# Kernel optimization log

Hardware: AMD Instinct MI355X
Metric: run time of the kernel (lower is better)

## Reference

```python
import jax, jax.numpy as jnp
import numpy as np

V = 5000      # output_class_dim
E = 512       # embed_dim
F = 512       # 2 * listener_hidden_dim
H = 512       # speller_hidden_dim
HEADS = 4
HD = F // HEADS  # 128
STEPS = 64    # max_label_len
B, T = 32, 1024


def setup_inputs() -> dict:
    key = jax.random.key(0)
    ks = jax.random.split(key, 10)
    s = 0.05
    return {
        "listener_feature": jax.random.normal(ks[0], (B, T, F), jnp.float32),
        "embedding": jax.random.normal(ks[1], (V, E), jnp.float32) * s,
        # LSTM cell (single layer, torch gate order i,f,g,o)
        "W_ih": jax.random.normal(ks[2], (4 * H, E + F), jnp.float32) * s,
        "W_hh": jax.random.normal(ks[3], (4 * H, H), jnp.float32) * s,
        "b_ih": jax.random.normal(ks[4], (4 * H,), jnp.float32) * s,
        "b_hh": jax.random.normal(ks[5], (4 * H,), jnp.float32) * s,
        # predict_hid: Linear(2H -> 512)
        "Wp": jax.random.normal(ks[6], (512, 2 * H), jnp.float32) * s,
        "bp": jax.random.normal(ks[7], (512,), jnp.float32) * s,
        # character_distribution: Linear(512 -> V)
        "Wc": jax.random.normal(ks[8], (V, 512), jnp.float32) * s,
        "bc": jax.random.normal(ks[9], (V,), jnp.float32) * s,
    }


def _decode(listener_feature, embedding, W_ih, W_hh, b_ih, b_hh, Wp, bp, Wc, bc):
    b = listener_feature.shape[0]
    lf_heads = listener_feature.reshape(b, T, HEADS, HD)  # [B,T,h,d]

    def lstm_cell(x, h, c):
        gates = x @ W_ih.T + h @ W_hh.T + (b_ih + b_hh)
        i, f, g, o = jnp.split(gates, 4, axis=-1)
        c_new = jax.nn.sigmoid(f) * c + jax.nn.sigmoid(i) * jnp.tanh(g)
        h_new = jax.nn.sigmoid(o) * jnp.tanh(c_new)
        return h_new, c_new

    def step(carry, _):
        h, c, rnn_in = carry
        h, c = lstm_cell(rnn_in, h, c)                       # rnn_output = h [B,H]
        ds = h.reshape(b, HEADS, HD)                          # decoder state per head
        energy = jnp.einsum('bhd,bthd->bht', ds, lf_heads)    # dot attention
        scores = jax.nn.softmax(energy, axis=-1)              # [B,h,T]
        context = jnp.einsum('bht,bthd->bhd', scores, lf_heads).reshape(b, F)
        concat = jnp.concatenate([h, context], axis=-1)       # [B,2H]
        hid = jnp.maximum(concat @ Wp.T + bp, 0.0)            # ReLU MLP
        raw_pred = jax.nn.log_softmax(hid @ Wc.T + bc, axis=-1)
        # greedy feedback (teacher_force_rate = 0 since ground_truth is None)
        tok = jnp.argmax(raw_pred, axis=-1)                   # [B]
        rnn_in_next = jnp.concatenate([embedding[tok], context], axis=-1)
        return (h, c, rnn_in_next), (raw_pred, scores[:, -1, :])

    h0 = jnp.zeros((b, H), listener_feature.dtype)
    c0 = jnp.zeros((b, H), listener_feature.dtype)
    # initial input: embedding of token 0, concat first listener frame
    emb0 = jnp.broadcast_to(embedding[0], (b, E))
    rnn_in0 = jnp.concatenate([emb0, listener_feature[:, 0, :]], axis=-1)

    _, (raw_pred_seq, attn_seq) = jax.lax.scan(step, (h0, c0, rnn_in0), None, length=STEPS)
    return raw_pred_seq, attn_seq  # [S,B,V], [S,B,T] (last head, as in original)


def reference(listener_feature, embedding, W_ih, W_hh, b_ih, b_hh, Wp, bp, Wc, bc):
    return _decode(listener_feature, embedding, W_ih, W_hh, b_ih, b_hh, Wp, bp, Wc, bc)
```

## Files before the change

### kernel.cpp

```cpp
#include <hip/hip_runtime.h>
#include <math.h>
#include <stdint.h>


#define NB 512
#define NT 256

constexpr int Tv = 1024, Vv = 5000, STEPS = 64;

constexpr int MCNT = 0;
constexpr int GEN  = 16;
constexpr int GCNT = 64;
constexpr int GFLG = 1024;
constexpr int ACNT = 2048;
constexpr int LCNT = 2560;
constexpr int WSU  = 4096;

constexpr int XH   = 0;
constexpr int HB   = XH + 32*1024;
constexpr int HID  = HB + 2*32*512;
constexpr int PART = HID + 32*512;
constexpr int E3   = PART + 32*4*16*130;
constexpr int PM   = E3 + 32*1024;
constexpr int PSUM = PM + 32*256;
constexpr int PIDX = PSUM + 32*256;
constexpr int MLS  = PIDX + 32*256;

__device__ __forceinline__ float sigm(float x) { return 1.f / (1.f + expf(-x)); }

__device__ __forceinline__ float ld4(const float* p) {
  return __hip_atomic_load(const_cast<float*>(p), __ATOMIC_RELAXED, __HIP_MEMORY_SCOPE_AGENT);
}
__device__ __forceinline__ float2 ld8(const float* p) {
  unsigned long long u = __hip_atomic_load(
      reinterpret_cast<unsigned long long*>(const_cast<float*>(p)),
      __ATOMIC_RELAXED, __HIP_MEMORY_SCOPE_AGENT);
  union { unsigned long long u; float2 f; } c; c.u = u; return c.f;
}
__device__ __forceinline__ int ld4i(const int* p) {
  return (int)__hip_atomic_load(reinterpret_cast<unsigned*>(const_cast<int*>(p)),
                                __ATOMIC_RELAXED, __HIP_MEMORY_SCOPE_AGENT);
}
__device__ __forceinline__ void st4(float* p, float v) {
  __hip_atomic_store(p, v, __ATOMIC_RELAXED, __HIP_MEMORY_SCOPE_AGENT);
}
__device__ __forceinline__ void st8(float* p, float2 v) {
  union { float2 f; unsigned long long u; } c; c.f = v;
  __hip_atomic_store(reinterpret_cast<unsigned long long*>(p), c.u,
                     __ATOMIC_RELAXED, __HIP_MEMORY_SCOPE_AGENT);
}
__device__ __forceinline__ void st4i(int* p, int v) {
  __hip_atomic_store(reinterpret_cast<unsigned*>(p), (unsigned)v,
                     __ATOMIC_RELAXED, __HIP_MEMORY_SCOPE_AGENT);
}
__device__ __forceinline__ unsigned ld_rlx(unsigned* p) {
  return __hip_atomic_load(p, __ATOMIC_RELAXED, __HIP_MEMORY_SCOPE_AGENT);
}
__device__ __forceinline__ void st_rlx(unsigned* p, unsigned v) {
  __hip_atomic_store(p, v, __ATOMIC_RELAXED, __HIP_MEMORY_SCOPE_AGENT);
}
__device__ __forceinline__ unsigned add_rlx(unsigned* p, unsigned v) {
  return __hip_atomic_fetch_add(p, v, __ATOMIC_RELAXED, __HIP_MEMORY_SCOPE_AGENT);
}

__device__ __forceinline__ void gsync(unsigned* wsu, int blk, int tid, unsigned& myGen) {
  __syncthreads();
  if (tid == 0) {
    const unsigned target = ++myGen;
    const int grp = blk >> 4;
    unsigned o = add_rlx(&wsu[GCNT + grp*16], 1u);
    if (o == target*16u - 1u) {
      unsigned o2 = add_rlx(&wsu[MCNT], 1u);
      if (o2 == target*32u - 1u) st_rlx(&wsu[GEN], target);
    }
    if ((blk & 15) == 0) {
      while (ld_rlx(&wsu[GEN]) != target) __builtin_amdgcn_s_sleep(8);
      st_rlx(&wsu[GFLG + grp*32], target);
    } else {
      while (ld_rlx(&wsu[GFLG + grp*32]) != target) __builtin_amdgcn_s_sleep(8);
    }
  }
  __syncthreads();
}

__global__ void speller_init(const float* __restrict__ LF, const float* __restrict__ Emb,
                             float* __restrict__ wsf, unsigned* __restrict__ wsu) {
  int b = blockIdx.x;
  for (int i = threadIdx.x; i < 512; i += NT) {
    st4(wsf + XH + b*1024 + i,       Emb[i]);
    st4(wsf + XH + b*1024 + 512 + i, LF[(size_t)b*Tv*512 + i]);
    st4(wsf + HB + b*512 + i,        0.f);
  }
  if (b == 0) for (int i = threadIdx.x; i < WSU; i += NT) st_rlx(wsu + i, 0u);
}

struct LdsA { float Wg[8][1536]; float Wpg[2][1536]; float gb[8]; float bpg[2]; };
struct LdsB { float Wc[20][512]; float bcl[20]; };
union  LdsU { LdsA a; LdsB b; };

__device__ __forceinline__ void gate_accum_A(float acc[8][2], float accW[2][2],
                                             const float* __restrict__ wsf,
                                             const float (&Wg)[8][1536],
                                             const float (&Wpg)[2][1536],
                                             int ks, int b0, int hbuf) {
#pragma unroll 2
  for (int q = 0; q < 8; ++q) {
    const int k4 = 512 + (q*16 + ks)*4;
    float2 xa[2], xb[2];
#pragma unroll
    for (int i = 0; i < 2; ++i) {
      const float* p = wsf + XH + (size_t)(b0+i)*1024 + k4;
      xa[i] = ld8(p); xb[i] = ld8(p + 2);
    }
#pragma unroll
    for (int r = 0; r < 8; ++r) {
      float4 wv = *(const float4*)(&Wg[r][k4]);
#pragma unroll
      for (int i = 0; i < 2; ++i)
        acc[r][i] += wv.x*xa[i].x + wv.y*xa[i].y + wv.z*xb[i].x + wv.w*xb[i].y;
    }
#pragma unroll
    for (int r = 0; r < 2; ++r) {
      float4 wv = *(const float4*)(&Wpg[r][k4]);
#pragma unroll
      for (int i = 0; i < 2; ++i)
        accW[r][i] += wv.x*xa[i].x + wv.y*xa[i].y + wv.z*xb[i].x + wv.w*xb[i].y;
    }
  }
#pragma unroll 2
  for (int q = 0; q < 8; ++q) {
    const int k4 = (q*16 + ks)*4;
    float2 xa[2], xb[2];
#pragma unroll
    for (int i = 0; i < 2; ++i) {
      const float* p = wsf + HB + hbuf*16384 + (size_t)(b0+i)*512 + k4;
      xa[i] = ld8(p); xb[i] = ld8(p + 2);
    }
#pragma unroll
    for (int r = 0; r < 8; ++r) {
      float4 wv = *(const float4*)(&Wg[r][1024 + k4]);
#pragma unroll
      for (int i = 0; i < 2; ++i)
        acc[r][i] += wv.x*xa[i].x + wv.y*xa[i].y + wv.z*xb[i].x + wv.w*xb[i].y;
    }
#pragma unroll
    for (int r = 0; r < 2; ++r) {
      float4 wv = *(const float4*)(&Wpg[r][1024 + k4]);
#pragma unroll
      for (int i = 0; i < 2; ++i)
        accW[r][i] += wv.x*xa[i].x + wv.y*xa[i].y + wv.z*xb[i].x + wv.w*xb[i].y;
    }
  }
}

__launch_bounds__(NT, 2)
__global__ void speller_main(const float* __restrict__ LF, const float* __restrict__ Emb,
                             const float* __restrict__ Wih, const float* __restrict__ Whh,
                             const float* __restrict__ bih, const float* __restrict__ bhh,
                             const float* __restrict__ Wp,  const float* __restrict__ bp,
                             const float* __restrict__ Wc,  const float* __restrict__ bc,
                             float* __restrict__ out, unsigned* __restrict__ wsu,
                             float* __restrict__ wsf) {
  const int blk = blockIdx.x, tid = threadIdx.x;
  unsigned myGen = 0;
  __shared__ LdsU lds;
  __shared__ float scr[784];
  __shared__ int  sint[300];

  const int ab = blk >> 4, atc = blk & 15;
  const int aw = tid >> 6, aln = tid & 63;

  float4 lfr[32];
  {
    const float4* src = (const float4*)(LF +
        (((size_t)ab*Tv + atc*64 + aln)*512 + aw*128));
#pragma unroll
    for (int q = 0; q < 32; ++q) lfr[q] = src[q];
  }

  if (blk < 256) {
    const int u0 = blk * 2;
    for (int idx = tid; idx < 8*1536; idx += NT) {
      int r = idx / 1536, k = idx - r*1536;
      int g = r >> 1, uu = r & 1;
      int row = g*512 + u0 + uu;
      lds.a.Wg[r][k] = (k < 1024) ? Wih[(size_t)row*1024 + k]
                                  : Whh[(size_t)row*512 + (k-1024)];
    }
    for (int idx = tid; idx < 2*1536; idx += NT) {
      int r = idx / 1536, k = idx - r*1536;
      float v = 0.f;
      if (k >= 512) v = (k < 1024) ? Wp[(size_t)(u0+r)*1024 + k]
                                   : Wp[(size_t)(u0+r)*1024 + (k-1024)];
      lds.a.Wpg[r][k] = v;
    }
    if (tid < 8) {
      int g = tid >> 1, uu = tid & 1, row = g*512 + u0 + uu;
      lds.a.gb[tid] = bih[row] + bhh[row];
    }
    if (tid < 2) lds.a.bpg[tid] = bp[u0 + tid];
  } else {
    const int blk2 = blk - 256, v0 = blk2*20;
    if (v0 < Vv) {
      for (int idx = tid; idx < 20*512; idx += NT) {
        int vi = idx >> 9, k = idx & 511;
        lds.b.Wc[vi][k] = Wc[(size_t)(v0+vi)*512 + k];
      }
      if (tid < 20) lds.b.bcl[tid] = bc[v0+tid];
    }
  }
  __syncthreads();

  float acc[8][2];
  float accW[2][2];
  float c_reg[2][2];
#pragma unroll
  for (int uu = 0; uu < 2; ++uu)
#pragma unroll
    for (int i = 0; i < 2; ++i) c_reg[uu][i] = 0.f;
  float lgv[20];

  if (blk < 256) {
    const int ks = tid & 15, b0 = (tid >> 4) * 2;
#pragma unroll
    for (int r = 0; r < 8; ++r)
#pragma unroll
      for (int i = 0; i < 2; ++i) acc[r][i] = 0.f;
#pragma unroll
    for (int r = 0; r < 2; ++r)
#pragma unroll
      for (int i = 0; i < 2; ++i) accW[r][i] = 0.f;
    gate_accum_A(acc, accW, wsf, lds.a.Wg, lds.a.Wpg, ks, b0, 0);
  }

#pragma unroll 1
  for (int s = 0; s < STEPS; ++s) {
    const int wbuf = (s + 1) & 1;

    if (blk < 256) {
      const int u0 = blk * 2;
      const int ks = tid & 15, b0 = (tid >> 4) * 2;
#pragma unroll 2
      for (int q = 0; q < 8; ++q) {
        const int k4 = (q*16 + ks)*4;
        float2 xa[2], xb[2];
#pragma unroll
        for (int i = 0; i < 2; ++i) {
          const float* p = wsf + XH + (size_t)(b0+i)*1024 + k4;
          xa[i] = ld8(p); xb[i] = ld8(p + 2);
        }
#pragma unroll
        for (int r = 0; r < 8; ++r) {
          float4 wv = *(const float4*)(&lds.a.Wg[r][k4]);
#pragma unroll
          for (int i = 0; i < 2; ++i)
            acc[r][i] += wv.x*xa[i].x + wv.y*xa[i].y + wv.z*xb[i].x + wv.w*xb[i].y;
        }
      }
#pragma unroll
      for (int r = 0; r < 8; ++r)
#pragma unroll
        for (int i = 0; i < 2; ++i) {
          float v = acc[r][i];
          v += __shfl_xor(v, 8); v += __shfl_xor(v, 4);
          v += __shfl_xor(v, 2); v += __shfl_xor(v, 1);
          acc[r][i] = v + lds.a.gb[r];
        }
      float hnew[2][2];
#pragma unroll
      for (int uu = 0; uu < 2; ++uu)
#pragma unroll
        for (int i = 0; i < 2; ++i) {
          float cn = sigm(acc[2+uu][i]) * c_reg[uu][i]
                   + sigm(acc[uu][i]) * tanhf(acc[4+uu][i]);
          c_reg[uu][i] = cn;
          hnew[uu][i] = sigm(acc[6+uu][i]) * tanhf(cn);
        }
      if (ks == 0) {
#pragma unroll
        for (int i = 0; i < 2; ++i)
          st8(wsf + HB + wbuf*16384 + (size_t)(b0+i)*512 + u0,
              make_float2(hnew[0][i], hnew[1][i]));
      }
    } else if (s > 0) {
      const int blk2 = blk - 256;
      if (blk2 < 250) {
        const int v0 = blk2 * 20, bb = tid >> 3, ks = tid & 7;
        if (ks == 0) {
          float2 ml = ld8(wsf + MLS + 2*bb);
          float sub = ml.x + ml.y;
#pragma unroll
          for (int vi = 0; vi < 20; ++vi)
            out[(size_t)(s-1)*160000 + (size_t)bb*5000 + v0 + vi] = lgv[vi] - sub;
        }
      }
    }
    gsync(wsu, blk, tid, myGen);

    {
      float* hs = scr;
      {
        float2 hv = ld8(wsf + HB + wbuf*16384 + (size_t)ab*512 + tid*2);
        hs[tid*2] = hv.x; hs[tid*2+1] = hv.y;
      }
      __syncthreads();
      float e = 0.f;
      {
        const float4* hp = (const float4*)(hs + aw*128);
#pragma unroll
        for (int q = 0; q < 32; ++q) {
          float4 f = lfr[q], hh = hp[q];
          e += f.x*hh.x + f.y*hh.y + f.z*hh.z + f.w*hh.w;
        }
      }
      float m = e;
#pragma unroll
      for (int off = 32; off; off >>= 1) m = fmaxf(m, __shfl_xor(m, off));
      float p = expf(e - m);
      float l = p;
#pragma unroll
      for (int off = 32; off; off >>= 1) l += __shfl_xor(l, off);
      if (aw == 3) st4(wsf + E3 + (size_t)ab*1024 + atc*64 + aln, e);
      float* pr = wsf + PART + (size_t)((ab*4 + aw)*16 + atc)*130;
#pragma unroll
      for (int ch = 0; ch < 2; ++ch) {
        float c[64];
#pragma unroll
        for (int q = 0; q < 16; ++q) {
          float4 f = lfr[ch*16 + q];
          c[4*q+0] = p*f.x; c[4*q+1] = p*f.y; c[4*q+2] = p*f.z; c[4*q+3] = p*f.w;
        }
#pragma unroll
        for (int o = 32; o >= 1; o >>= 1) {
#pragma unroll
          for (int j = 0; j < 32; ++j) {
            if (j < o) {
              float keep = (aln & o) ? c[j + o] : c[j];
              float send = (aln & o) ? c[j] : c[j + o];
              c[j] = keep + __shfl_xor(send, o);
            }
          }
        }
        st4(pr + 2 + ch*64 + aln, c[0]);
      }
      if (aln == 0) st8(pr, make_float2(m, l));
      __syncthreads();
      if (tid == 0) {
        unsigned old = add_rlx(&wsu[ACNT + ab*16], 1u);
        sint[0] = (old == (unsigned)(s*16 + 15));
      }
      __syncthreads();
      if (sint[0]) {
        const int w2 = tid >> 6, ln2 = tid & 63;
        const float* pb = wsf + PART + (size_t)(ab*4 + w2)*16*130;
        float M = -1e30f;
        float mv[16], lv[16];
#pragma unroll
        for (int i = 0; i < 16; ++i) { float2 t = ld8(pb + i*130); mv[i] = t.x; lv[i] = t.y; M = fmaxf(M, t.x); }
        float L = 0.f;
        float sc[16];
#pragma unroll
        for (int i = 0; i < 16; ++i) { sc[i] = expf(mv[i] - M); L += lv[i] * sc[i]; }
        float cc0 = 0.f, cc1 = 0.f;
#pragma unroll
        for (int i = 0; i < 16; ++i) {
          float2 cx = ld8(pb + i*130 + 2 + 2*ln2);
          cc0 += sc[i]*cx.x; cc1 += sc[i]*cx.y;
        }
        float invL = 1.f / L;
        st8(wsf + XH + (size_t)ab*1024 + 512 + w2*128 + 2*ln2,
            make_float2(cc0*invL, cc1*invL));
        if (ln2 == 0) { scr[768 + w2*2] = M; scr[769 + w2*2] = L; }
        __syncthreads();
        float M3 = scr[768 + 6], iL3 = 1.f / scr[768 + 7];
        for (int i = tid; i < 1024; i += NT)
          out[(size_t)10240000 + ((size_t)(s*32 + ab))*1024 + i] =
              expf(ld4(wsf + E3 + (size_t)ab*1024 + i) - M3) * iL3;
      }
    }
    gsync(wsu, blk, tid, myGen);

    if (blk < 256) {
      const int ks = tid & 15, b0 = (tid >> 4) * 2;
#pragma unroll
      for (int r = 0; r < 8; ++r)
#pragma unroll
        for (int i = 0; i < 2; ++i) acc[r][i] = 0.f;
#pragma unroll
      for (int r = 0; r < 2; ++r)
#pragma unroll
        for (int i = 0; i < 2; ++i) accW[r][i] = 0.f;
      gate_accum_A(acc, accW, wsf, lds.a.Wg, lds.a.Wpg, ks, b0, wbuf);
#pragma unroll
      for (int r = 0; r < 2; ++r)
#pragma unroll
        for (int i = 0; i < 2; ++i) {
          float v = accW[r][i];
          v += __shfl_xor(v, 8); v += __shfl_xor(v, 4);
          v += __shfl_xor(v, 2); v += __shfl_xor(v, 1);
          accW[r][i] = v + lds.a.bpg[r];
        }
      if (ks == 0) {
#pragma unroll
        for (int i = 0; i < 2; ++i)
          st8(wsf + HID + (size_t)(b0+i)*512 + blk*2,
              make_float2(fmaxf(accW[0][i], 0.f), fmaxf(accW[1][i], 0.f)));
      }
    }
    gsync(wsu, blk, tid, myGen);

    if (blk >= 256) {
      const int blk2 = blk - 256;
      if (blk2 < 250) {
        const int v0 = blk2 * 20;
        const int bb = tid >> 3, ks = tid & 7;
#pragma unroll
        for (int vi = 0; vi < 20; ++vi) lgv[vi] = 0.f;
        const float* hb = wsf + HID + (size_t)bb*512;
#pragma unroll 1
        for (int half = 0; half < 2; ++half) {
          float4 xr[8];
#pragma unroll
          for (int q = 0; q < 8; ++q) {
            const float* p = hb + ((half*8 + q)*8 + ks)*4;
            float2 a = ld8(p), b2v = ld8(p + 2);
            xr[q] = make_float4(a.x, a.y, b2v.x, b2v.y);
          }
#pragma unroll
          for (int vi = 0; vi < 20; ++vi) {
            float a = 0.f;
#pragma unroll
            for (int q = 0; q < 8; ++q) {
              float4 wv = *(const float4*)(&lds.b.Wc[vi][((half*8 + q)*8 + ks)*4]);
              a += wv.x*xr[q].x + wv.y*xr[q].y + wv.z*xr[q].z + wv.w*xr[q].w;
            }
            lgv[vi] += a;
          }
        }
#pragma unroll
        for (int vi = 0; vi < 20; ++vi) {
          float a = lgv[vi];
          a += __shfl_xor(a, 1); a += __shfl_xor(a, 2); a += __shfl_xor(a, 4);
          lgv[vi] = a + lds.b.bcl[vi];
        }
        float mych = lgv[0]; int ami = 0;
#pragma unroll
        for (int vi = 1; vi < 20; ++vi)
          if (lgv[vi] > mych) { mych = lgv[vi]; ami = vi; }
        float sume = 0.f;
#pragma unroll
        for (int vi = 0; vi < 20; ++vi) sume += expf(lgv[vi] - mych);
        if (ks == 0) {
          st4(wsf + PM + bb*256 + blk2, mych);
          st4(wsf + PSUM + bb*256 + blk2, sume);
          st4i((int*)(wsf + PIDX) + bb*256 + blk2, v0 + ami);
        }
      }
      __syncthreads();
      if (tid == 0 && blk2 < 250) add_rlx(&wsu[LCNT], 1u);
      if (blk2 < 32) {
        const int b2 = blk2;
        if (tid == 0) {
          while (ld_rlx(&wsu[LCNT]) < (unsigned)((s + 1) * 250))
            __builtin_amdgcn_s_sleep(8);
        }
        __syncthreads();
        float mv = -1e30f, sv = 0.f; int iv = 0x7fffffff;
        if (tid < 250) {
          mv = ld4(wsf + PM + b2*256 + tid);
          sv = ld4(wsf + PSUM + b2*256 + tid);
          iv = ld4i((const int*)(wsf + PIDX) + b2*256 + tid);
        }
        scr[tid] = mv; sint[40 + tid] = iv;
        __syncthreads();
        for (int off = 128; off; off >>= 1) {
          if (tid < off) {
            float m2 = scr[tid + off]; int i2 = sint[40 + tid + off];
            if (m2 > scr[tid] || (m2 == scr[tid] && i2 < sint[40 + tid])) {
              scr[tid] = m2; sint[40 + tid] = i2;
            }
          }
          __syncthreads();
        }
        float M = scr[0]; int tok = sint[40];
        __syncthreads();
        scr[tid] = sv * expf(mv - M);
        __syncthreads();
        for (int off = 128; off; off >>= 1) {
          if (tid < off) scr[tid] += scr[tid + off];
          __syncthreads();
        }
        if (tid == 0) st8(wsf + MLS + 2*b2, make_float2(M, logf(scr[0])));
        for (int i = tid; i < 256; i += NT) {
          const float2* er = (const float2*)(Emb + (size_t)tok*512);
          st8(wsf + XH + (size_t)b2*1024 + 2*i, er[i]);
        }
      }
    }
    gsync(wsu, blk, tid, myGen);
  }

  if (blk >= 256) {
    const int blk2 = blk - 256;
    if (blk2 < 250) {
      const int v0 = blk2 * 20, bb = tid >> 3, ks = tid & 7;
      if (ks == 0) {
        float2 ml = ld8(wsf + MLS + 2*bb);
        float sub = ml.x + ml.y;
#pragma unroll
        for (int vi = 0; vi < 20; ++vi)
          out[(size_t)63*160000 + (size_t)bb*5000 + v0 + vi] = lgv[vi] - sub;
      }
    }
  }
}

extern "C" void kernel_launch(void* const* d_in, const int* in_sizes, int n_in,
                              void* d_out, int out_size, void* d_ws, size_t ws_size,
                              hipStream_t stream) {
  (void)in_sizes; (void)n_in; (void)out_size; (void)ws_size;
  const float* LF  = (const float*)d_in[0];
  const float* Emb = (const float*)d_in[1];
  const float* Wih = (const float*)d_in[2];
  const float* Whh = (const float*)d_in[3];
  const float* bih = (const float*)d_in[4];
  const float* bhh = (const float*)d_in[5];
  const float* Wp  = (const float*)d_in[6];
  const float* bp  = (const float*)d_in[7];
  const float* Wc  = (const float*)d_in[8];
  const float* bc  = (const float*)d_in[9];
  float* out = (float*)d_out;
  unsigned* wsu = (unsigned*)d_ws;
  float* wsf = (float*)d_ws + WSU;

  speller_init<<<32, NT, 0, stream>>>(LF, Emb, wsf, wsu);
  speller_main<<<NB, NT, 0, stream>>>(LF, Emb, Wih, Whh, bih, bhh, Wp, bp, Wc, bc,
                                      out, wsu, wsf);
}
```

Measured before the change: 5.857 ms.

## Halve persistent grid to 256 blocks of 512 threads, doubling per-block work

```diff
diff --git a/kernel.cpp b/kernel.cpp
--- a/kernel.cpp
+++ b/kernel.cpp
@@ -3,8 +3,8 @@
 #include <stdint.h>
 
 
-#define NB 512
-#define NT 256
+#define NB 256
+#define NT 512
 
 constexpr int Tv = 1024, Vv = 5000, STEPS = 64;
 
@@ -71,7 +71,7 @@
     unsigned o = add_rlx(&wsu[GCNT + grp*16], 1u);
     if (o == target*16u - 1u) {
       unsigned o2 = add_rlx(&wsu[MCNT], 1u);
-      if (o2 == target*32u - 1u) st_rlx(&wsu[GEN], target);
+      if (o2 == target*16u - 1u) st_rlx(&wsu[GEN], target);
     }
     if ((blk & 15) == 0) {
       while (ld_rlx(&wsu[GEN]) != target) __builtin_amdgcn_s_sleep(8);
@@ -86,74 +86,58 @@
 __global__ void speller_init(const float* __restrict__ LF, const float* __restrict__ Emb,
                              float* __restrict__ wsf, unsigned* __restrict__ wsu) {
   int b = blockIdx.x;
-  for (int i = threadIdx.x; i < 512; i += NT) {
+  for (int i = threadIdx.x; i < 512; i += 256) {
     st4(wsf + XH + b*1024 + i,       Emb[i]);
     st4(wsf + XH + b*1024 + 512 + i, LF[(size_t)b*Tv*512 + i]);
     st4(wsf + HB + b*512 + i,        0.f);
   }
-  if (b == 0) for (int i = threadIdx.x; i < WSU; i += NT) st_rlx(wsu + i, 0u);
-}
-
-struct LdsA { float Wg[8][1536]; float Wpg[2][1536]; float gb[8]; float bpg[2]; };
-struct LdsB { float Wc[20][512]; float bcl[20]; };
+  if (b == 0) for (int i = threadIdx.x; i < WSU; i += 256) st_rlx(wsu + i, 0u);
+}
+
+struct LdsA { float Wg[16][1536]; float Wpg[4][1536]; float gb[16]; float bpg[4]; };
+struct LdsB { float Wc[40][512]; float bcl[40]; };
 union  LdsU { LdsA a; LdsB b; };
 
-__device__ __forceinline__ void gate_accum_A(float acc[8][2], float accW[2][2],
+__device__ __forceinline__ void gate_accum_A(float acc[16], float accW[4],
                                              const float* __restrict__ wsf,
-                                             const float (&Wg)[8][1536],
-                                             const float (&Wpg)[2][1536],
-                                             int ks, int b0, int hbuf) {
+                                             const float (&Wg)[16][1536],
+                                             const float (&Wpg)[4][1536],
+                                             int ks, int b, int hbuf) {
 #pragma unroll 2
   for (int q = 0; q < 8; ++q) {
     const int k4 = 512 + (q*16 + ks)*4;
-    float2 xa[2], xb[2];
-#pragma unroll
-    for (int i = 0; i < 2; ++i) {
-      const float* p = wsf + XH + (size_t)(b0+i)*1024 + k4;
-      xa[i] = ld8(p); xb[i] = ld8(p + 2);
-    }
-#pragma unroll
-    for (int r = 0; r < 8; ++r) {
+    const float* p = wsf + XH + (size_t)b*1024 + k4;
+    float2 xa = ld8(p), xb = ld8(p + 2);
+#pragma unroll
+    for (int r = 0; r < 16; ++r) {
       float4 wv = *(const float4*)(&Wg[r][k4]);
-#pragma unroll
-      for (int i = 0; i < 2; ++i)
-        acc[r][i] += wv.x*xa[i].x + wv.y*xa[i].y + wv.z*xb[i].x + wv.w*xb[i].y;
-    }
-#pragma unroll
-    for (int r = 0; r < 2; ++r) {
+      acc[r] += wv.x*xa.x + wv.y*xa.y + wv.z*xb.x + wv.w*xb.y;
+    }
+#pragma unroll
+    for (int r = 0; r < 4; ++r) {
       float4 wv = *(const float4*)(&Wpg[r][k4]);
-#pragma unroll
-      for (int i = 0; i < 2; ++i)
-        accW[r][i] += wv.x*xa[i].x + wv.y*xa[i].y + wv.z*xb[i].x + wv.w*xb[i].y;
+      accW[r] += wv.x*xa.x + wv.y*xa.y + wv.z*xb.x + wv.w*xb.y;
     }
   }
 #pragma unroll 2
   for (int q = 0; q < 8; ++q) {
     const int k4 = (q*16 + ks)*4;
-    float2 xa[2], xb[2];
-#pragma unroll
-    for (int i = 0; i < 2; ++i) {
-      const float* p = wsf + HB + hbuf*16384 + (size_t)(b0+i)*512 + k4;
-      xa[i] = ld8(p); xb[i] = ld8(p + 2);
-    }
-#pragma unroll
-    for (int r = 0; r < 8; ++r) {
+    const float* p = wsf + HB + hbuf*16384 + (size_t)b*512 + k4;
+    float2 xa = ld8(p), xb = ld8(p + 2);
+#pragma unroll
+    for (int r = 0; r < 16; ++r) {
       float4 wv = *(const float4*)(&Wg[r][1024 + k4]);
-#pragma unroll
-      for (int i = 0; i < 2; ++i)
-        acc[r][i] += wv.x*xa[i].x + wv.y*xa[i].y + wv.z*xb[i].x + wv.w*xb[i].y;
-    }
-#pragma unroll
-    for (int r = 0; r < 2; ++r) {
+      acc[r] += wv.x*xa.x + wv.y*xa.y + wv.z*xb.x + wv.w*xb.y;
+    }
+#pragma unroll
+    for (int r = 0; r < 4; ++r) {
       float4 wv = *(const float4*)(&Wpg[r][1024 + k4]);
-#pragma unroll
-      for (int i = 0; i < 2; ++i)
-        accW[r][i] += wv.x*xa[i].x + wv.y*xa[i].y + wv.z*xb[i].x + wv.w*xb[i].y;
-    }
-  }
-}
-
-__launch_bounds__(NT, 2)
+      accW[r] += wv.x*xa.x + wv.y*xa.y + wv.z*xb.x + wv.w*xb.y;
+    }
+  }
+}
+
+__launch_bounds__(NT, 1)
 __global__ void speller_main(const float* __restrict__ LF, const float* __restrict__ Emb,
                              const float* __restrict__ Wih, const float* __restrict__ Whh,
                              const float* __restrict__ bih, const float* __restrict__ bhh,
@@ -167,8 +151,10 @@
   __shared__ float scr[784];
   __shared__ int  sint[300];
 
-  const int ab = blk >> 4, atc = blk & 15;
-  const int aw = tid >> 6, aln = tid & 63;
+  const int ab  = blk >> 3;
+  const int wavid = tid >> 6, aln = tid & 63;
+  const int aw  = wavid & 3, sub = wavid >> 2;
+  const int atc = (blk & 7)*2 + sub;
 
   float4 lfr[32];
   {
@@ -178,120 +164,104 @@
     for (int q = 0; q < 32; ++q) lfr[q] = src[q];
   }
 
-  if (blk < 256) {
-    const int u0 = blk * 2;
-    for (int idx = tid; idx < 8*1536; idx += NT) {
+  if (blk < 128) {
+    const int u0 = blk * 4;
+    for (int idx = tid; idx < 16*1536; idx += NT) {
       int r = idx / 1536, k = idx - r*1536;
-      int g = r >> 1, uu = r & 1;
+      int g = r >> 2, uu = r & 3;
       int row = g*512 + u0 + uu;
       lds.a.Wg[r][k] = (k < 1024) ? Wih[(size_t)row*1024 + k]
                                   : Whh[(size_t)row*512 + (k-1024)];
     }
-    for (int idx = tid; idx < 2*1536; idx += NT) {
+    for (int idx = tid; idx < 4*1536; idx += NT) {
       int r = idx / 1536, k = idx - r*1536;
       float v = 0.f;
       if (k >= 512) v = (k < 1024) ? Wp[(size_t)(u0+r)*1024 + k]
                                    : Wp[(size_t)(u0+r)*1024 + (k-1024)];
       lds.a.Wpg[r][k] = v;
     }
-    if (tid < 8) {
-      int g = tid >> 1, uu = tid & 1, row = g*512 + u0 + uu;
+    if (tid < 16) {
+      int g = tid >> 2, uu = tid & 3, row = g*512 + u0 + uu;
       lds.a.gb[tid] = bih[row] + bhh[row];
     }
-    if (tid < 2) lds.a.bpg[tid] = bp[u0 + tid];
+    if (tid < 4) lds.a.bpg[tid] = bp[u0 + tid];
   } else {
-    const int blk2 = blk - 256, v0 = blk2*20;
-    if (v0 < Vv) {
-      for (int idx = tid; idx < 20*512; idx += NT) {
+    const int blk2 = blk - 128, v0 = blk2*40;
+    if (blk2 < 125) {
+      for (int idx = tid; idx < 40*512; idx += NT) {
         int vi = idx >> 9, k = idx & 511;
         lds.b.Wc[vi][k] = Wc[(size_t)(v0+vi)*512 + k];
       }
-      if (tid < 20) lds.b.bcl[tid] = bc[v0+tid];
+      if (tid < 40) lds.b.bcl[tid] = bc[v0+tid];
     }
   }
   __syncthreads();
 
-  float acc[8][2];
-  float accW[2][2];
-  float c_reg[2][2];
-#pragma unroll
-  for (int uu = 0; uu < 2; ++uu)
-#pragma unroll
-    for (int i = 0; i < 2; ++i) c_reg[uu][i] = 0.f;
-  float lgv[20];
-
-  if (blk < 256) {
-    const int ks = tid & 15, b0 = (tid >> 4) * 2;
-#pragma unroll
-    for (int r = 0; r < 8; ++r)
-#pragma unroll
-      for (int i = 0; i < 2; ++i) acc[r][i] = 0.f;
-#pragma unroll
-    for (int r = 0; r < 2; ++r)
-#pragma unroll
-      for (int i = 0; i < 2; ++i) accW[r][i] = 0.f;
-    gate_accum_A(acc, accW, wsf, lds.a.Wg, lds.a.Wpg, ks, b0, 0);
+  float acc[16];
+  float accW[4];
+  float c_reg[4];
+#pragma unroll
+  for (int uu = 0; uu < 4; ++uu) c_reg[uu] = 0.f;
+  float lgv[40];
+
+  if (blk < 128) {
+    const int ks = tid & 15, b = tid >> 4;
+#pragma unroll
+    for (int r = 0; r < 16; ++r) acc[r] = 0.f;
+#pragma unroll
+    for (int r = 0; r < 4; ++r) accW[r] = 0.f;
+    gate_accum_A(acc, accW, wsf, lds.a.Wg, lds.a.Wpg, ks, b, 0);
   }
 
 #pragma unroll 1
   for (int s = 0; s < STEPS; ++s) {
     const int wbuf = (s + 1) & 1;
 
-    if (blk < 256) {
-      const int u0 = blk * 2;
-      const int ks = tid & 15, b0 = (tid >> 4) * 2;
+    if (blk < 128) {
+      const int u0 = blk * 4;
+      const int ks = tid & 15, b = tid >> 4;
 #pragma unroll 2
       for (int q = 0; q < 8; ++q) {
         const int k4 = (q*16 + ks)*4;
-        float2 xa[2], xb[2];
-#pragma unroll
-        for (int i = 0; i < 2; ++i) {
-          const float* p = wsf + XH + (size_t)(b0+i)*1024 + k4;
-          xa[i] = ld8(p); xb[i] = ld8(p + 2);
-        }
-#pragma unroll
-        for (int r = 0; r < 8; ++r) {
+        const float* p = wsf + XH + (size_t)b*1024 + k4;
+        float2 xa = ld8(p), xb = ld8(p + 2);
+#pragma unroll
+        for (int r = 0; r < 16; ++r) {
           float4 wv = *(const float4*)(&lds.a.Wg[r][k4]);
-#pragma unroll
-          for (int i = 0; i < 2; ++i)
-            acc[r][i] += wv.x*xa[i].x + wv.y*xa[i].y + wv.z*xb[i].x + wv.w*xb[i].y;
-        }
-      }
-#pragma unroll
-      for (int r = 0; r < 8; ++r)
-#pragma unroll
-        for (int i = 0; i < 2; ++i) {
-          float v = acc[r][i];
-          v += __shfl_xor(v, 8); v += __shfl_xor(v, 4);
-          v += __shfl_xor(v, 2); v += __shfl_xor(v, 1);
-          acc[r][i] = v + lds.a.gb[r];
-        }
-      float hnew[2][2];
-#pragma unroll
-      for (int uu = 0; uu < 2; ++uu)
-#pragma unroll
-        for (int i = 0; i < 2; ++i) {
-          float cn = sigm(acc[2+uu][i]) * c_reg[uu][i]
-                   + sigm(acc[uu][i]) * tanhf(acc[4+uu][i]);
-          c_reg[uu][i] = cn;
-          hnew[uu][i] = sigm(acc[6+uu][i]) * tanhf(cn);
-        }
+          acc[r] += wv.x*xa.x + wv.y*xa.y + wv.z*xb.x + wv.w*xb.y;
+        }
+      }
+#pragma unroll
+      for (int r = 0; r < 16; ++r) {
+        float v = acc[r];
+        v += __shfl_xor(v, 8); v += __shfl_xor(v, 4);
+        v += __shfl_xor(v, 2); v += __shfl_xor(v, 1);
+        acc[r] = v + lds.a.gb[r];
+      }
+      float hnew[4];
+#pragma unroll
+      for (int uu = 0; uu < 4; ++uu) {
+        float cn = sigm(acc[4+uu]) * c_reg[uu]
+                 + sigm(acc[uu]) * tanhf(acc[8+uu]);
+        c_reg[uu] = cn;
+        hnew[uu] = sigm(acc[12+uu]) * tanhf(cn);
+      }
       if (ks == 0) {
-#pragma unroll
-        for (int i = 0; i < 2; ++i)
-          st8(wsf + HB + wbuf*16384 + (size_t)(b0+i)*512 + u0,
-              make_float2(hnew[0][i], hnew[1][i]));
+        st8(wsf + HB + wbuf*16384 + (size_t)b*512 + u0,
+            make_float2(hnew[0], hnew[1]));
+        st8(wsf + HB + wbuf*16384 + (size_t)b*512 + u0 + 2,
+            make_float2(hnew[2], hnew[3]));
       }
     } else if (s > 0) {
-      const int blk2 = blk - 256;
-      if (blk2 < 250) {
-        const int v0 = blk2 * 20, bb = tid >> 3, ks = tid & 7;
+      const int blk2 = blk - 128;
+      if (blk2 < 125) {
+        const int v0 = blk2 * 40, bb = tid >> 4, ks = tid & 15;
         if (ks == 0) {
           float2 ml = ld8(wsf + MLS + 2*bb);
-          float sub = ml.x + ml.y;
-#pragma unroll
-          for (int vi = 0; vi < 20; ++vi)
-            out[(size_t)(s-1)*160000 + (size_t)bb*5000 + v0 + vi] = lgv[vi] - sub;
+          float sub2 = ml.x + ml.y;
+#pragma unroll
+          for (int vi = 0; vi < 40; ++vi)
+            out[(size_t)(s-1)*160000 + (size_t)bb*5000 + v0 + vi] = lgv[vi] - sub2;
         }
       }
     }
@@ -299,7 +269,7 @@
 
     {
       float* hs = scr;
-      {
+      if (tid < 256) {
         float2 hv = ld8(wsf + HB + wbuf*16384 + (size_t)ab*512 + tid*2);
         hs[tid*2] = hv.x; hs[tid*2+1] = hv.y;
       }
@@ -347,30 +317,32 @@
       __syncthreads();
       if (tid == 0) {
         unsigned old = add_rlx(&wsu[ACNT + ab*16], 1u);
-        sint[0] = (old == (unsigned)(s*16 + 15));
+        sint[0] = (old == (unsigned)(s*8 + 7));
       }
       __syncthreads();
       if (sint[0]) {
-        const int w2 = tid >> 6, ln2 = tid & 63;
-        const float* pb = wsf + PART + (size_t)(ab*4 + w2)*16*130;
-        float M = -1e30f;
-        float mv[16], lv[16];
-#pragma unroll
-        for (int i = 0; i < 16; ++i) { float2 t = ld8(pb + i*130); mv[i] = t.x; lv[i] = t.y; M = fmaxf(M, t.x); }
-        float L = 0.f;
-        float sc[16];
-#pragma unroll
-        for (int i = 0; i < 16; ++i) { sc[i] = expf(mv[i] - M); L += lv[i] * sc[i]; }
-        float cc0 = 0.f, cc1 = 0.f;
-#pragma unroll
-        for (int i = 0; i < 16; ++i) {
-          float2 cx = ld8(pb + i*130 + 2 + 2*ln2);
-          cc0 += sc[i]*cx.x; cc1 += sc[i]*cx.y;
-        }
-        float invL = 1.f / L;
-        st8(wsf + XH + (size_t)ab*1024 + 512 + w2*128 + 2*ln2,
-            make_float2(cc0*invL, cc1*invL));
-        if (ln2 == 0) { scr[768 + w2*2] = M; scr[769 + w2*2] = L; }
+        if (tid < 256) {
+          const int w2 = tid >> 6, ln2 = tid & 63;
+          const float* pb = wsf + PART + (size_t)(ab*4 + w2)*16*130;
+          float M = -1e30f;
+          float mv[16], lv[16];
+#pragma unroll
+          for (int i = 0; i < 16; ++i) { float2 t = ld8(pb + i*130); mv[i] = t.x; lv[i] = t.y; M = fmaxf(M, t.x); }
+          float L = 0.f;
+          float sc[16];
+#pragma unroll
+          for (int i = 0; i < 16; ++i) { sc[i] = expf(mv[i] - M); L += lv[i] * sc[i]; }
+          float cc0 = 0.f, cc1 = 0.f;
+#pragma unroll
+          for (int i = 0; i < 16; ++i) {
+            float2 cx = ld8(pb + i*130 + 2 + 2*ln2);
+            cc0 += sc[i]*cx.x; cc1 += sc[i]*cx.y;
+          }
+          float invL = 1.f / L;
+          st8(wsf + XH + (size_t)ab*1024 + 512 + w2*128 + 2*ln2,
+              make_float2(cc0*invL, cc1*invL));
+          if (ln2 == 0) { scr[768 + w2*2] = M; scr[769 + w2*2] = L; }
+        }
         __syncthreads();
         float M3 = scr[768 + 6], iL3 = 1.f / scr[768 + 7];
         for (int i = tid; i < 1024; i += NT)
@@ -380,76 +352,62 @@
     }
     gsync(wsu, blk, tid, myGen);
 
-    if (blk < 256) {
-      const int ks = tid & 15, b0 = (tid >> 4) * 2;
-#pragma unroll
-      for (int r = 0; r < 8; ++r)
-#pragma unroll
-        for (int i = 0; i < 2; ++i) acc[r][i] = 0.f;
-#pragma unroll
-      for (int r = 0; r < 2; ++r)
-#pragma unroll
-        for (int i = 0; i < 2; ++i) accW[r][i] = 0.f;
-      gate_accum_A(acc, accW, wsf, lds.a.Wg, lds.a.Wpg, ks, b0, wbuf);
-#pragma unroll
-      for (int r = 0; r < 2; ++r)
-#pragma unroll
-        for (int i = 0; i < 2; ++i) {
-          float v = accW[r][i];
-          v += __shfl_xor(v, 8); v += __shfl_xor(v, 4);
-          v += __shfl_xor(v, 2); v += __shfl_xor(v, 1);
-          accW[r][i] = v + lds.a.bpg[r];
-        }
+    if (blk < 128) {
+      const int u0 = blk * 4;
+      const int ks = tid & 15, b = tid >> 4;
+#pragma unroll
+      for (int r = 0; r < 16; ++r) acc[r] = 0.f;
+#pragma unroll
+      for (int r = 0; r < 4; ++r) accW[r] = 0.f;
+      gate_accum_A(acc, accW, wsf, lds.a.Wg, lds.a.Wpg, ks, b, wbuf);
+#pragma unroll
+      for (int r = 0; r < 4; ++r) {
+        float v = accW[r];
+        v += __shfl_xor(v, 8); v += __shfl_xor(v, 4);
+        v += __shfl_xor(v, 2); v += __shfl_xor(v, 1);
+        accW[r] = v + lds.a.bpg[r];
+      }
       if (ks == 0) {
-#pragma unroll
-        for (int i = 0; i < 2; ++i)
-          st8(wsf + HID + (size_t)(b0+i)*512 + blk*2,
-              make_float2(fmaxf(accW[0][i], 0.f), fmaxf(accW[1][i], 0.f)));
+        st8(wsf + HID + (size_t)b*512 + u0,
+            make_float2(fmaxf(accW[0], 0.f), fmaxf(accW[1], 0.f)));
+        st8(wsf + HID + (size_t)b*512 + u0 + 2,
+            make_float2(fmaxf(accW[2], 0.f), fmaxf(accW[3], 0.f)));
       }
     }
     gsync(wsu, blk, tid, myGen);
 
-    if (blk >= 256) {
-      const int blk2 = blk - 256;
-      if (blk2 < 250) {
-        const int v0 = blk2 * 20;
-        const int bb = tid >> 3, ks = tid & 7;
-#pragma unroll
-        for (int vi = 0; vi < 20; ++vi) lgv[vi] = 0.f;
+    if (blk >= 128) {
+      const int blk2 = blk - 128;
+      if (blk2 < 125) {
+        const int v0 = blk2 * 40;
+        const int bb = tid >> 4, ks = tid & 15;
         const float* hb = wsf + HID + (size_t)bb*512;
-#pragma unroll 1
-        for (int half = 0; half < 2; ++half) {
-          float4 xr[8];
+        float4 xr[8];
+#pragma unroll
+        for (int q = 0; q < 8; ++q) {
+          const float* p = hb + (q*16 + ks)*4;
+          float2 a = ld8(p), b2v = ld8(p + 2);
+          xr[q] = make_float4(a.x, a.y, b2v.x, b2v.y);
+        }
+#pragma unroll
+        for (int vi = 0; vi < 40; ++vi) {
+          float a = 0.f;
 #pragma unroll
           for (int q = 0; q < 8; ++q) {
-            const float* p = hb + ((half*8 + q)*8 + ks)*4;
-            float2 a = ld8(p), b2v = ld8(p + 2);
-            xr[q] = make_float4(a.x, a.y, b2v.x, b2v.y);
+            float4 wv = *(const float4*)(&lds.b.Wc[vi][(q*16 + ks)*4]);
+            a += wv.x*xr[q].x + wv.y*xr[q].y + wv.z*xr[q].z + wv.w*xr[q].w;
           }
-#pragma unroll
-          for (int vi = 0; vi < 20; ++vi) {
-            float a = 0.f;
-#pragma unroll
-            for (int q = 0; q < 8; ++q) {
-              float4 wv = *(const float4*)(&lds.b.Wc[vi][((half*8 + q)*8 + ks)*4]);
-              a += wv.x*xr[q].x + wv.y*xr[q].y + wv.z*xr[q].z + wv.w*xr[q].w;
-            }
-            lgv[vi] += a;
-          }
-        }
-#pragma unroll
-        for (int vi = 0; vi < 20; ++vi) {
-          float a = lgv[vi];
-          a += __shfl_xor(a, 1); a += __shfl_xor(a, 2); a += __shfl_xor(a, 4);
+          a += __shfl_xor(a, 1); a += __shfl_xor(a, 2);
+          a += __shfl_xor(a, 4); a += __shfl_xor(a, 8);
           lgv[vi] = a + lds.b.bcl[vi];
         }
         float mych = lgv[0]; int ami = 0;
 #pragma unroll
-        for (int vi = 1; vi < 20; ++vi)
+        for (int vi = 1; vi < 40; ++vi)
           if (lgv[vi] > mych) { mych = lgv[vi]; ami = vi; }
         float sume = 0.f;
 #pragma unroll
-        for (int vi = 0; vi < 20; ++vi) sume += expf(lgv[vi] - mych);
+        for (int vi = 0; vi < 40; ++vi) sume += expf(lgv[vi] - mych);
         if (ks == 0) {
           st4(wsf + PM + bb*256 + blk2, mych);
           st4(wsf + PSUM + bb*256 + blk2, sume);
@@ -457,21 +415,21 @@
         }
       }
       __syncthreads();
-      if (tid == 0 && blk2 < 250) add_rlx(&wsu[LCNT], 1u);
+      if (tid == 0 && blk2 < 125) add_rlx(&wsu[LCNT], 1u);
       if (blk2 < 32) {
         const int b2 = blk2;
         if (tid == 0) {
-          while (ld_rlx(&wsu[LCNT]) < (unsigned)((s + 1) * 250))
+          while (ld_rlx(&wsu[LCNT]) < (unsigned)((s + 1) * 125))
             __builtin_amdgcn_s_sleep(8);
         }
         __syncthreads();
         float mv = -1e30f, sv = 0.f; int iv = 0x7fffffff;
-        if (tid < 250) {
+        if (tid < 125) {
           mv = ld4(wsf + PM + b2*256 + tid);
           sv = ld4(wsf + PSUM + b2*256 + tid);
           iv = ld4i((const int*)(wsf + PIDX) + b2*256 + tid);
         }
-        scr[tid] = mv; sint[40 + tid] = iv;
+        if (tid < 256) { scr[tid] = mv; sint[40 + tid] = iv; }
         __syncthreads();
         for (int off = 128; off; off >>= 1) {
           if (tid < off) {
@@ -484,7 +442,7 @@
         }
         float M = scr[0]; int tok = sint[40];
         __syncthreads();
-        scr[tid] = sv * expf(mv - M);
+        if (tid < 256) scr[tid] = sv * expf(mv - M);
         __syncthreads();
         for (int off = 128; off; off >>= 1) {
           if (tid < off) scr[tid] += scr[tid + off];
@@ -500,16 +458,16 @@
     gsync(wsu, blk, tid, myGen);
   }
 
-  if (blk >= 256) {
-    const int blk2 = blk - 256;
-    if (blk2 < 250) {
-      const int v0 = blk2 * 20, bb = tid >> 3, ks = tid & 7;
+  if (blk >= 128) {
+    const int blk2 = blk - 128;
+    if (blk2 < 125) {
+      const int v0 = blk2 * 40, bb = tid >> 4, ks = tid & 15;
       if (ks == 0) {
         float2 ml = ld8(wsf + MLS + 2*bb);
-        float sub = ml.x + ml.y;
-#pragma unroll
-        for (int vi = 0; vi < 20; ++vi)
-          out[(size_t)63*160000 + (size_t)bb*5000 + v0 + vi] = lgv[vi] - sub;
+        float sub2 = ml.x + ml.y;
+#pragma unroll
+        for (int vi = 0; vi < 40; ++vi)
+          out[(size_t)63*160000 + (size_t)bb*5000 + v0 + vi] = lgv[vi] - sub2;
       }
     }
   }
@@ -533,7 +491,7 @@
   unsigned* wsu = (unsigned*)d_ws;
   float* wsf = (float*)d_ws + WSU;
 
-  speller_init<<<32, NT, 0, stream>>>(LF, Emb, wsf, wsu);
+  speller_init<<<32, 256, 0, stream>>>(LF, Emb, wsf, wsu);
   speller_main<<<NB, NT, 0, stream>>>(LF, Emb, Wih, Whh, bih, bhh, Wp, bp, Wc, bc,
                                       out, wsu, wsf);
 }
```

Measured after the change: 6.017 ms. 2.7% more time.

## Publish greedy token via flag and overlap embedding gate GEMV with vocab phase

Applied to the files above, without the earlier changes.

```diff
diff --git a/kernel.cpp b/kernel.cpp
--- a/kernel.cpp
+++ b/kernel.cpp
@@ -14,6 +14,7 @@
 constexpr int GFLG = 1024;
 constexpr int ACNT = 2048;
 constexpr int LCNT = 2560;
+constexpr int TOKF = 2576;
 constexpr int WSU  = 4096;
 
 constexpr int XH   = 0;
@@ -86,12 +87,12 @@
 __global__ void speller_init(const float* __restrict__ LF, const float* __restrict__ Emb,
                              float* __restrict__ wsf, unsigned* __restrict__ wsu) {
   int b = blockIdx.x;
-  for (int i = threadIdx.x; i < 512; i += NT) {
-    st4(wsf + XH + b*1024 + i,       Emb[i]);
+  (void)Emb;
+  for (int i = threadIdx.x; i < 512; i += 256) {
     st4(wsf + XH + b*1024 + 512 + i, LF[(size_t)b*Tv*512 + i]);
     st4(wsf + HB + b*512 + i,        0.f);
   }
-  if (b == 0) for (int i = threadIdx.x; i < WSU; i += NT) st_rlx(wsu + i, 0u);
+  if (b == 0) for (int i = threadIdx.x; i < WSU; i += 256) st_rlx(wsu + i, 0u);
 }
 
 struct LdsA { float Wg[8][1536]; float Wpg[2][1536]; float gb[8]; float bpg[2]; };
@@ -230,6 +231,17 @@
     for (int r = 0; r < 2; ++r)
 #pragma unroll
       for (int i = 0; i < 2; ++i) accW[r][i] = 0.f;
+#pragma unroll 2
+    for (int q = 0; q < 8; ++q) {
+      const int k4 = (q*16 + ks)*4;
+      float4 xe = *(const float4*)(Emb + k4);
+#pragma unroll
+      for (int r = 0; r < 8; ++r) {
+        float4 wv = *(const float4*)(&lds.a.Wg[r][k4]);
+        float d = wv.x*xe.x + wv.y*xe.y + wv.z*xe.z + wv.w*xe.w;
+        acc[r][0] += d; acc[r][1] += d;
+      }
+    }
     gate_accum_A(acc, accW, wsf, lds.a.Wg, lds.a.Wpg, ks, b0, 0);
   }
 
@@ -240,23 +252,6 @@
     if (blk < 256) {
       const int u0 = blk * 2;
       const int ks = tid & 15, b0 = (tid >> 4) * 2;
-#pragma unroll 2
-      for (int q = 0; q < 8; ++q) {
-        const int k4 = (q*16 + ks)*4;
-        float2 xa[2], xb[2];
-#pragma unroll
-        for (int i = 0; i < 2; ++i) {
-          const float* p = wsf + XH + (size_t)(b0+i)*1024 + k4;
-          xa[i] = ld8(p); xb[i] = ld8(p + 2);
-        }
-#pragma unroll
-        for (int r = 0; r < 8; ++r) {
-          float4 wv = *(const float4*)(&lds.a.Wg[r][k4]);
-#pragma unroll
-          for (int i = 0; i < 2; ++i)
-            acc[r][i] += wv.x*xa[i].x + wv.y*xa[i].y + wv.z*xb[i].x + wv.w*xb[i].y;
-        }
-      }
 #pragma unroll
       for (int r = 0; r < 8; ++r)
 #pragma unroll
@@ -483,6 +478,8 @@
           __syncthreads();
         }
         float M = scr[0]; int tok = sint[40];
+        if (tid == 0)
+          st_rlx(&wsu[TOKF + b2*16], ((unsigned)(s + 1) << 13) | (unsigned)tok);
         __syncthreads();
         scr[tid] = sv * expf(mv - M);
         __syncthreads();
@@ -491,9 +488,30 @@
           __syncthreads();
         }
         if (tid == 0) st8(wsf + MLS + 2*b2, make_float2(M, logf(scr[0])));
-        for (int i = tid; i < 256; i += NT) {
-          const float2* er = (const float2*)(Emb + (size_t)tok*512);
-          st8(wsf + XH + (size_t)b2*1024 + 2*i, er[i]);
+      }
+    } else if (s < 63) {
+      if (tid < 32) {
+        unsigned u = ld_rlx(&wsu[TOKF + tid*16]);
+        while ((u >> 13) != (unsigned)(s + 1)) {
+          __builtin_amdgcn_s_sleep(2);
+          u = ld_rlx(&wsu[TOKF + tid*16]);
+        }
+        sint[100 + tid] = (int)(u & 8191u);
+      }
+      __syncthreads();
+      const int ks = tid & 15, b0 = (tid >> 4) * 2;
+      const float* e0 = Emb + (size_t)sint[100 + b0]     * 512;
+      const float* e1 = Emb + (size_t)sint[100 + b0 + 1] * 512;
+#pragma unroll 2
+      for (int q = 0; q < 8; ++q) {
+        const int k4 = (q*16 + ks)*4;
+        float4 xa = *(const float4*)(e0 + k4);
+        float4 xb = *(const float4*)(e1 + k4);
+#pragma unroll
+        for (int r = 0; r < 8; ++r) {
+          float4 wv = *(const float4*)(&lds.a.Wg[r][k4]);
+          acc[r][0] += wv.x*xa.x + wv.y*xa.y + wv.z*xa.z + wv.w*xa.w;
+          acc[r][1] += wv.x*xb.x + wv.y*xb.y + wv.z*xb.z + wv.w*xb.w;
         }
       }
     }
@@ -533,7 +551,7 @@
   unsigned* wsu = (unsigned*)d_ws;
   float* wsf = (float*)d_ws + WSU;
 
-  speller_init<<<32, NT, 0, stream>>>(LF, Emb, wsf, wsu);
+  speller_init<<<32, 256, 0, stream>>>(LF, Emb, wsf, wsu);
   speller_main<<<NB, NT, 0, stream>>>(LF, Emb, Wih, Whh, bih, bhh, Wp, bp, Wc, bc,
                                       out, wsu, wsf);
 }
```

Result: slower. 6.534 ms (+11.6%).
